# Performance work log

Hardware: AMD Instinct MI355X
Metric: run time of the kernel (lower is better)

Reference implementation:

```python
import jax, jax.numpy as jnp
import numpy as np

NUM_HEADS = 16
HIDDEN = 1024
TOTAL = 2048
NSEG = 8


def setup_inputs() -> dict:
    key = jax.random.key(0)
    ks = jax.random.split(key, 10)
    x = jax.random.normal(ks[0], (TOTAL, HIDDEN), dtype=jnp.float32)
    # cu_seqlens: [0, b1, ..., TOTAL], sorted segment boundaries
    inner = np.sort(np.random.default_rng(0).integers(1, TOTAL, size=NSEG - 1))
    cu_seqlens = jnp.asarray(np.concatenate([[0], inner, [TOTAL]]), dtype=jnp.int32)
    s = 1.0 / np.sqrt(HIDDEN)
    def lin(k):
        kw, kb = jax.random.split(k)
        W = jax.random.uniform(kw, (HIDDEN, HIDDEN), jnp.float32, -s, s)
        b = jax.random.uniform(kb, (HIDDEN,), jnp.float32, -s, s)
        return W, b
    Wq, bq = lin(ks[1]); Wk, bk = lin(ks[2]); Wv, bv = lin(ks[3]); Wo, bo = lin(ks[4])
    return {"hidden_states_packed": x, "cu_seqlens": cu_seqlens,
            "Wq": Wq, "bq": bq, "Wk": Wk, "bk": bk,
            "Wv": Wv, "bv": bv, "Wo": Wo, "bo": bo}


def reference(hidden_states_packed, cu_seqlens, Wq, bq, Wk, bk, Wv, bv, Wo, bo):
    T, H = hidden_states_packed.shape
    dh = H // NUM_HEADS
    x = hidden_states_packed
    q = (x @ Wq.T + bq).reshape(T, NUM_HEADS, dh)
    k = (x @ Wk.T + bk).reshape(T, NUM_HEADS, dh)
    v = (x @ Wv.T + bv).reshape(T, NUM_HEADS, dh)
    # segment id of each token from cu_seqlens boundaries
    seg = jnp.searchsorted(cu_seqlens, jnp.arange(T, dtype=jnp.int32), side="right")
    same_seg = seg[:, None] == seg[None, :]  # [T, T] block-diagonal mask
    scale = 1.0 / jnp.sqrt(jnp.asarray(dh, x.dtype))
    scores = jnp.einsum("qhd,khd->hqk", q, k) * scale  # [H, T, T]
    neg = jnp.asarray(jnp.finfo(scores.dtype).min, scores.dtype)
    scores = jnp.where(same_seg[None, :, :], scores, neg)
    attn = jax.nn.softmax(scores, axis=-1)
    ctx = jnp.einsum("hqk,khd->qhd", attn, v).reshape(T, H)
    return ctx @ Wo.T + bo
```

## Files before the change

kernel.cpp:

```cpp
#include <hip/hip_runtime.h>

typedef _Float16 f16x8 __attribute__((ext_vector_type(8)));
typedef _Float16 f16x4 __attribute__((ext_vector_type(4)));
typedef float    f32x4 __attribute__((ext_vector_type(4)));

#define MFMA_F16(a, b, c) __builtin_amdgcn_mfma_f32_16x16x32_f16((a), (b), (c), 0, 0, 0)

typedef __attribute__((address_space(1))) void gas_void;
typedef __attribute__((address_space(3))) void las_void;
#define GLOAD_LDS16(g, l) \
  __builtin_amdgcn_global_load_lds((gas_void*)(g), (las_void*)(l), 16, 0, 0)

#define NEG_INF (-__builtin_inff())

constexpr int T_SEQ  = 2048;
constexpr int HID    = 1024;
constexpr int NHEADS = 16;
constexpr int DH     = 64;
constexpr int NSEG   = 8;

__global__ __launch_bounds__(256) void convert_all(
    const float* __restrict__ x,
    const float* __restrict__ Wq, const float* __restrict__ Wk,
    const float* __restrict__ Wv, const float* __restrict__ Wo,
    _Float16* __restrict__ xh,
    _Float16* __restrict__ Wqh, _Float16* __restrict__ Wkh,
    _Float16* __restrict__ Wvh, _Float16* __restrict__ Woh) {
  int i = blockIdx.x * 256 + threadIdx.x;
  const float* src;
  _Float16* dst;
  int local;
  if (i < 524288) {
    src = x; dst = xh; local = i;
  } else {
    int j = i - 524288;
    int w = j >> 18;
    local = j & 262143;
    src = (w == 0) ? Wq : (w == 1) ? Wk : (w == 2) ? Wv : Wo;
    dst = (w == 0) ? Wqh : (w == 1) ? Wkh : (w == 2) ? Wvh : Woh;
  }
  float4 f = *(const float4*)(src + (size_t)local * 4);
  f16x4 h;
  h[0] = (_Float16)f.x; h[1] = (_Float16)f.y;
  h[2] = (_Float16)f.z; h[3] = (_Float16)f.w;
  *(f16x4*)(dst + (size_t)local * 4) = h;
}

template <int LAYOUT, int BM>
__device__ __forceinline__ void gemm128(const _Float16* __restrict__ A,
                                        const _Float16* __restrict__ B,
                                        const float* __restrict__ bias,
                                        _Float16* __restrict__ outh,
                                        float* __restrict__ outf) {
  constexpr int K = HID, N = HID;
  constexpr int MI = BM / 32;
  constexpr int LA = (BM * 8) / 512;
  __shared__ _Float16 As[BM * 64];
  __shared__ _Float16 Bs[128 * 64];
  const int tid  = threadIdx.x;
  const int wave = tid >> 6, lane = tid & 63;
  const int lr = lane & 15, lq = lane >> 4;
  const int wm = (wave >> 2) * (BM / 2);
  const int wn = (wave & 3) * 32;
  const int bm = blockIdx.y * BM, bn = blockIdx.x * 128;

  const _Float16* gA[LA > 0 ? LA : 1];
  const _Float16* gB[2];
  _Float16* lA[LA > 0 ? LA : 1];
  _Float16* lB[2];
#pragma unroll
  for (int i = 0; i < LA; ++i) {
    const int s = i * 512 + tid;
    const int row = s >> 3, pch = s & 7;
    const int lch = pch ^ (row & 7);
    gA[i] = A + (size_t)(bm + row) * K + lch * 8;
    lA[i] = &As[(i * 512 + wave * 64) * 8];
  }
#pragma unroll
  for (int i = 0; i < 2; ++i) {
    const int s = i * 512 + tid;
    const int row = s >> 3, pch = s & 7;
    const int lch = pch ^ (row & 7);
    gB[i] = B + (size_t)(bn + row) * K + lch * 8;
    lB[i] = &Bs[(i * 512 + wave * 64) * 8];
  }

  f32x4 acc[MI][2] = {};

  for (int kk = 0; kk < K; kk += 64) {
#pragma unroll
    for (int i = 0; i < LA; ++i) GLOAD_LDS16(gA[i] + kk, lA[i]);
#pragma unroll
    for (int i = 0; i < 2; ++i) GLOAD_LDS16(gB[i] + kk, lB[i]);
    __syncthreads();
#pragma unroll
    for (int ks = 0; ks < 2; ++ks) {
      f16x8 af[MI], bf[2];
#pragma unroll
      for (int mi = 0; mi < MI; ++mi) {
        const int row = wm + mi * 16 + lr;
        af[mi] = *(const f16x8*)&As[row * 64 + (((ks * 4 + lq) ^ (row & 7)) * 8)];
      }
#pragma unroll
      for (int ni = 0; ni < 2; ++ni) {
        const int row = wn + ni * 16 + lr;
        bf[ni] = *(const f16x8*)&Bs[row * 64 + (((ks * 4 + lq) ^ (row & 7)) * 8)];
      }
#pragma unroll
      for (int mi = 0; mi < MI; ++mi)
#pragma unroll
        for (int ni = 0; ni < 2; ++ni)
          acc[mi][ni] = MFMA_F16(af[mi], bf[ni], acc[mi][ni]);
    }
    __syncthreads();
  }

#pragma unroll
  for (int ni = 0; ni < 2; ++ni) {
    const int col = bn + wn + ni * 16 + lr;
    const float bv = bias[col];
#pragma unroll
    for (int mi = 0; mi < MI; ++mi) {
      const f32x4 v = acc[mi][ni];
      const int row0 = bm + wm + mi * 16 + lq * 4;
      if (LAYOUT == 3) {
        f16x4 o;
#pragma unroll
        for (int r = 0; r < 4; ++r) o[r] = (_Float16)(v[r] + bv);
        *(f16x4*)&outh[(size_t)col * T_SEQ + row0] = o;
      } else {
#pragma unroll
        for (int r = 0; r < 4; ++r) {
          const int row = row0 + r;
          const float val = v[r] + bv;
          if (LAYOUT == 0)
            outh[((size_t)(col >> 6) * T_SEQ + row) * DH + (col & 63)] = (_Float16)val;
          else
            outf[(size_t)row * N + col] = val;
        }
      }
    }
  }
}

__global__ __launch_bounds__(512) void gemm_qkv(
    const _Float16* __restrict__ xh,
    const _Float16* __restrict__ Wqh, const _Float16* __restrict__ Wkh,
    const _Float16* __restrict__ Wvh,
    const float* __restrict__ bq, const float* __restrict__ bk,
    const float* __restrict__ bv,
    _Float16* __restrict__ qp, _Float16* __restrict__ kp,
    _Float16* __restrict__ vT) {
  const int z = blockIdx.z;
  if (z == 0) {
    gemm128<0, 128>(xh, Wqh, bq, qp, nullptr);
  } else if (z == 1) {
    gemm128<0, 128>(xh, Wkh, bk, kp, nullptr);
  } else {
    gemm128<3, 128>(xh, Wvh, bv, vT, nullptr);
  }
}

__global__ __launch_bounds__(512) void gemm_out(
    const _Float16* __restrict__ ctxh, const _Float16* __restrict__ Woh,
    const float* __restrict__ bo, float* __restrict__ out) {
  gemm128<1, 64>(ctxh, Woh, bo, nullptr, out);
}

__device__ __forceinline__ float redsum16(float v) {
  v += __shfl_xor(v, 1);
  v += __shfl_xor(v, 2);
  v += __shfl_xor(v, 4);
  v += __shfl_xor(v, 8);
  return v;
}

__global__ __launch_bounds__(512, 4) void attn_kernel(
    const _Float16* __restrict__ qp, const _Float16* __restrict__ kp,
    const _Float16* __restrict__ vT, const int* __restrict__ cu,
    _Float16* __restrict__ ctx) {
  constexpr float SCL2E = 0.125f * 1.44269504f;
  constexpr int PSTR = 72;
  __shared__ _Float16 Ks[2][64 * 64];
  __shared__ _Float16 Vs[2][64 * 64];
  __shared__ _Float16 Pl[8][16 * PSTR];
  __shared__ float mO[4][16][64];
  __shared__ float mL[4][16];
  const int h  = blockIdx.y;
  const int q0 = blockIdx.x * 64;
  const int tid = threadIdx.x, wave = tid >> 6, lane = tid & 63;
  const int lr = lane & 15, lq = lane >> 4;
  const int qsub = wave & 3, khalf = wave >> 2;
  const int qw = q0 + qsub * 16;

  int cs[NSEG + 1];
#pragma unroll
  for (int i = 0; i <= NSEG; ++i) cs[i] = cu[i];

  int sstart[4], send[4];
#pragma unroll
  for (int r = 0; r < 4; ++r) {
    const int row = qw + lq * 4 + r;
    sstart[r] = 0; send[r] = T_SEQ;
#pragma unroll
    for (int s = 0; s < NSEG; ++s)
      if (row >= cs[s] && row < cs[s + 1]) { sstart[r] = cs[s]; send[r] = cs[s + 1]; }
  }
  int klo = 0, khi = T_SEQ;
#pragma unroll
  for (int s = 0; s < NSEG; ++s) {
    if (q0 >= cs[s] && q0 < cs[s + 1]) klo = cs[s];
    if (q0 + 63 >= cs[s] && q0 + 63 < cs[s + 1]) khi = cs[s + 1];
  }
  klo &= ~63;
  const int range  = khi - klo;
  const int hlen   = ((range + 127) >> 7) << 6;
  const int nsteps = hlen >> 6;
  const int kstart = klo + khalf * hlen;

  const _Float16* qbase = qp + ((size_t)h * T_SEQ + qw + lr) * DH;
  const f16x8 qf0 = *(const f16x8*)(qbase + lq * 8);
  const f16x8 qf1 = *(const f16x8*)(qbase + 32 + lq * 8);

  const _Float16* kb = kp + (size_t)h * T_SEQ * DH;
  const _Float16* vb = vT + (size_t)h * DH * T_SEQ;

  const int ht = qsub * 64 + lane;
  int kRow[2], kCol[2], vRow[2], vCol[2];
  _Float16* lK[2];
  _Float16* lV[2];
#pragma unroll
  for (int i = 0; i < 2; ++i) {
    const int s = i * 256 + ht;
    const int row = s >> 3, pch = s & 7;
    const int lch = pch ^ (row & 7);
    kRow[i] = row; kCol[i] = lch * 8;
    vRow[i] = row; vCol[i] = lch * 8;
    lK[i] = &Ks[khalf][(i * 256 + qsub * 64) * 8];
    lV[i] = &Vs[khalf][(i * 256 + qsub * 64) * 8];
  }

  float lst[4] = {0.f, 0.f, 0.f, 0.f};
  f32x4 oacc[4];
#pragma unroll
  for (int c = 0; c < 4; ++c) oacc[c] = f32x4{0.f, 0.f, 0.f, 0.f};

  _Float16* pw = &Pl[wave][0];

  for (int s = 0; s < nsteps; ++s) {
    const int kt = kstart + s * 64;
#pragma unroll
    for (int i = 0; i < 2; ++i) {
      const int grow = min(kt + kRow[i], T_SEQ - 1);
      GLOAD_LDS16(kb + (size_t)grow * DH + kCol[i], lK[i]);
    }
#pragma unroll
    for (int i = 0; i < 2; ++i) {
      const int gcol = min(kt + vCol[i], T_SEQ - 8);
      GLOAD_LDS16(vb + (size_t)vRow[i] * T_SEQ + gcol, lV[i]);
    }
    __syncthreads();

    f32x4 sc[4];
#pragma unroll
    for (int n = 0; n < 4; ++n) {
      const int row = n * 16 + lr;
      const f16x8 kf0 =
          *(const f16x8*)&Ks[khalf][row * 64 + (((0 * 4 + lq) ^ (row & 7)) * 8)];
      const f16x8 kf1 =
          *(const f16x8*)&Ks[khalf][row * 64 + (((1 * 4 + lq) ^ (row & 7)) * 8)];
      sc[n] = f32x4{0.f, 0.f, 0.f, 0.f};
      sc[n] = MFMA_F16(qf0, kf0, sc[n]);
      sc[n] = MFMA_F16(qf1, kf1, sc[n]);
    }
#pragma unroll
    for (int r = 0; r < 4; ++r) {
      float p[4];
#pragma unroll
      for (int n = 0; n < 4; ++n) {
        const int col = kt + n * 16 + lr;
        const float vv =
            (col >= sstart[r] && col < send[r]) ? sc[n][r] * SCL2E : NEG_INF;
        p[n] = exp2f(vv);
      }
      lst[r] += (p[0] + p[1]) + (p[2] + p[3]);
      _Float16* pr = &pw[(lq * 4 + r) * PSTR + lr];
      pr[0]  = (_Float16)p[0];
      pr[16] = (_Float16)p[1];
      pr[32] = (_Float16)p[2];
      pr[48] = (_Float16)p[3];
    }
    const f16x8 pf0 = *(const f16x8*)&pw[lr * PSTR + lq * 8];
    const f16x8 pf1 = *(const f16x8*)&pw[lr * PSTR + 32 + lq * 8];
#pragma unroll
    for (int c = 0; c < 4; ++c) {
      const int row = c * 16 + lr;
      const f16x8 vf0 =
          *(const f16x8*)&Vs[khalf][row * 64 + (((0 * 4 + lq) ^ (row & 7)) * 8)];
      const f16x8 vf1 =
          *(const f16x8*)&Vs[khalf][row * 64 + (((1 * 4 + lq) ^ (row & 7)) * 8)];
      oacc[c] = MFMA_F16(pf0, vf0, oacc[c]);
      oacc[c] = MFMA_F16(pf1, vf1, oacc[c]);
    }
    __syncthreads();
  }

#pragma unroll
  for (int r = 0; r < 4; ++r) lst[r] = redsum16(lst[r]);

  if (khalf) {
#pragma unroll
    for (int c = 0; c < 4; ++c)
#pragma unroll
      for (int r = 0; r < 4; ++r)
        mO[qsub][lq * 4 + r][c * 16 + lr] = oacc[c][r];
    if (lr == 0) {
#pragma unroll
      for (int r = 0; r < 4; ++r) mL[qsub][lq * 4 + r] = lst[r];
    }
  }
  __syncthreads();
  if (!khalf) {
#pragma unroll
    for (int r = 0; r < 4; ++r) lst[r] += mL[qsub][lq * 4 + r];
#pragma unroll
    for (int c = 0; c < 4; ++c)
#pragma unroll
      for (int r = 0; r < 4; ++r) {
        const int row = qw + lq * 4 + r;
        const float val =
            (oacc[c][r] + mO[qsub][lq * 4 + r][c * 16 + lr]) / lst[r];
        ctx[(size_t)row * HID + h * DH + c * 16 + lr] = (_Float16)val;
      }
  }
}

extern "C" void kernel_launch(void* const* d_in, const int* in_sizes, int n_in,
                              void* d_out, int out_size, void* d_ws, size_t ws_size,
                              hipStream_t stream) {
  const float* x  = (const float*)d_in[0];
  const int* cu   = (const int*)d_in[1];
  const float* Wq = (const float*)d_in[2]; const float* bq = (const float*)d_in[3];
  const float* Wk = (const float*)d_in[4]; const float* bk = (const float*)d_in[5];
  const float* Wv = (const float*)d_in[6]; const float* bv = (const float*)d_in[7];
  const float* Wo = (const float*)d_in[8]; const float* bo = (const float*)d_in[9];
  float* out = (float*)d_out;

  char* ws = (char*)d_ws;
  _Float16* xh   = (_Float16*)(ws + (size_t)0);
  _Float16* Wqh  = (_Float16*)(ws + ((size_t)4 << 20));
  _Float16* Wkh  = (_Float16*)(ws + ((size_t)6 << 20));
  _Float16* Wvh  = (_Float16*)(ws + ((size_t)8 << 20));
  _Float16* Woh  = (_Float16*)(ws + ((size_t)10 << 20));
  _Float16* qp   = (_Float16*)(ws + ((size_t)12 << 20));
  _Float16* kp   = (_Float16*)(ws + ((size_t)16 << 20));
  _Float16* vT   = (_Float16*)(ws + ((size_t)20 << 20));
  _Float16* ctxh = (_Float16*)(ws + ((size_t)24 << 20));

  convert_all<<<6144, 256, 0, stream>>>(x, Wq, Wk, Wv, Wo, xh, Wqh, Wkh, Wvh, Woh);
  gemm_qkv<<<dim3(8, 16, 3), 512, 0, stream>>>(xh, Wqh, Wkh, Wvh, bq, bk, bv, qp, kp, vT);
  attn_kernel<<<dim3(T_SEQ / 64, NHEADS), 512, 0, stream>>>(qp, kp, vT, cu, ctxh);
  gemm_out<<<dim3(8, 32), 512, 0, stream>>>(ctxh, Woh, bo, out);
}
```

Measured before the change: 141.7 us.

## Split GEMM K dimension across wave halves with LDS reduction

Restructures the projection GEMMs into an intra-block split-K: the 8 waves split into two groups that each process half of K with their own LDS tiles. Each wave now computes a larger 2x2-quadrant tile (4 N fragments instead of 2), which raises MFMA work per LDS fragment load. The partial sums are reduced through shared memory before the bias add and store. Launch bounds now request 4 blocks per CU. The cost is a larger LDS footprint, an extra reduction and barrier, and more accumulator registers per wave.

```diff
diff --git a/kernel.cpp b/kernel.cpp
--- a/kernel.cpp
+++ b/kernel.cpp
@@ -47,103 +47,129 @@
 }
 
 template <int LAYOUT, int BM>
-__device__ __forceinline__ void gemm128(const _Float16* __restrict__ A,
+__device__ __forceinline__ void gemm_sk(const _Float16* __restrict__ A,
                                         const _Float16* __restrict__ B,
                                         const float* __restrict__ bias,
                                         _Float16* __restrict__ outh,
                                         float* __restrict__ outf) {
-  constexpr int K = HID, N = HID;
-  constexpr int MI = BM / 32;
-  constexpr int LA = (BM * 8) / 512;
-  __shared__ _Float16 As[BM * 64];
-  __shared__ _Float16 Bs[128 * 64];
+  constexpr int K = HID, N = HID, KH = K / 2;
+  constexpr int QM = BM / 2;
+  constexpr int MI = QM / 16;
+  constexpr int LA = BM / 32;
+  __shared__ _Float16 SMEM[2 * BM * 64 + 2 * 128 * 64];
+  _Float16* As = SMEM;
+  _Float16* Bs = SMEM + 2 * BM * 64;
   const int tid  = threadIdx.x;
   const int wave = tid >> 6, lane = tid & 63;
   const int lr = lane & 15, lq = lane >> 4;
-  const int wm = (wave >> 2) * (BM / 2);
-  const int wn = (wave & 3) * 32;
+  const int kh = wave >> 2, q = wave & 3;
+  const int wm = (q >> 1) * QM, wn = (q & 1) * 64;
   const int bm = blockIdx.y * BM, bn = blockIdx.x * 128;
 
-  const _Float16* gA[LA > 0 ? LA : 1];
-  const _Float16* gB[2];
-  _Float16* lA[LA > 0 ? LA : 1];
-  _Float16* lB[2];
+  const int hl = q * 64 + lane;
+  const _Float16* gA[LA];
+  const _Float16* gB[4];
+  _Float16* lA[LA];
+  _Float16* lB[4];
 #pragma unroll
   for (int i = 0; i < LA; ++i) {
-    const int s = i * 512 + tid;
+    const int s = i * 256 + hl;
     const int row = s >> 3, pch = s & 7;
     const int lch = pch ^ (row & 7);
-    gA[i] = A + (size_t)(bm + row) * K + lch * 8;
-    lA[i] = &As[(i * 512 + wave * 64) * 8];
-  }
-#pragma unroll
-  for (int i = 0; i < 2; ++i) {
-    const int s = i * 512 + tid;
+    gA[i] = A + (size_t)(bm + row) * K + kh * KH + lch * 8;
+    lA[i] = &As[(kh * BM * 64) + (i * 256 + q * 64) * 8];
+  }
+#pragma unroll
+  for (int i = 0; i < 4; ++i) {
+    const int s = i * 256 + hl;
     const int row = s >> 3, pch = s & 7;
     const int lch = pch ^ (row & 7);
-    gB[i] = B + (size_t)(bn + row) * K + lch * 8;
-    lB[i] = &Bs[(i * 512 + wave * 64) * 8];
-  }
-
-  f32x4 acc[MI][2] = {};
-
-  for (int kk = 0; kk < K; kk += 64) {
+    gB[i] = B + (size_t)(bn + row) * K + kh * KH + lch * 8;
+    lB[i] = &Bs[(kh * 128 * 64) + (i * 256 + q * 64) * 8];
+  }
+
+  f32x4 acc[MI][4] = {};
+
+  for (int kk = 0; kk < KH; kk += 64) {
 #pragma unroll
     for (int i = 0; i < LA; ++i) GLOAD_LDS16(gA[i] + kk, lA[i]);
 #pragma unroll
-    for (int i = 0; i < 2; ++i) GLOAD_LDS16(gB[i] + kk, lB[i]);
+    for (int i = 0; i < 4; ++i) GLOAD_LDS16(gB[i] + kk, lB[i]);
     __syncthreads();
 #pragma unroll
     for (int ks = 0; ks < 2; ++ks) {
-      f16x8 af[MI], bf[2];
+      f16x8 af[MI], bf[4];
 #pragma unroll
       for (int mi = 0; mi < MI; ++mi) {
         const int row = wm + mi * 16 + lr;
-        af[mi] = *(const f16x8*)&As[row * 64 + (((ks * 4 + lq) ^ (row & 7)) * 8)];
-      }
-#pragma unroll
-      for (int ni = 0; ni < 2; ++ni) {
+        af[mi] = *(const f16x8*)&As[(kh * BM * 64) + row * 64 +
+                                    (((ks * 4 + lq) ^ (row & 7)) * 8)];
+      }
+#pragma unroll
+      for (int ni = 0; ni < 4; ++ni) {
         const int row = wn + ni * 16 + lr;
-        bf[ni] = *(const f16x8*)&Bs[row * 64 + (((ks * 4 + lq) ^ (row & 7)) * 8)];
+        bf[ni] = *(const f16x8*)&Bs[(kh * 128 * 64) + row * 64 +
+                                    (((ks * 4 + lq) ^ (row & 7)) * 8)];
       }
 #pragma unroll
       for (int mi = 0; mi < MI; ++mi)
 #pragma unroll
-        for (int ni = 0; ni < 2; ++ni)
+        for (int ni = 0; ni < 4; ++ni)
           acc[mi][ni] = MFMA_F16(af[mi], bf[ni], acc[mi][ni]);
     }
     __syncthreads();
   }
 
-#pragma unroll
-  for (int ni = 0; ni < 2; ++ni) {
-    const int col = bn + wn + ni * 16 + lr;
-    const float bv = bias[col];
-#pragma unroll
-    for (int mi = 0; mi < MI; ++mi) {
-      const f32x4 v = acc[mi][ni];
-      const int row0 = bm + wm + mi * 16 + lq * 4;
-      if (LAYOUT == 3) {
-        f16x4 o;
-#pragma unroll
-        for (int r = 0; r < 4; ++r) o[r] = (_Float16)(v[r] + bv);
-        *(f16x4*)&outh[(size_t)col * T_SEQ + row0] = o;
-      } else {
-#pragma unroll
-        for (int r = 0; r < 4; ++r) {
-          const int row = row0 + r;
-          const float val = v[r] + bv;
-          if (LAYOUT == 0)
-            outh[((size_t)(col >> 6) * T_SEQ + row) * DH + (col & 63)] = (_Float16)val;
-          else
-            outf[(size_t)row * N + col] = val;
+  float* mbuf = (float*)SMEM;
+  if (kh) {
+#pragma unroll
+    for (int mi = 0; mi < MI; ++mi)
+#pragma unroll
+      for (int ni = 0; ni < 4; ++ni)
+        *(f32x4*)&mbuf[(((q * 64 + lane) * MI * 4) + mi * 4 + ni) * 4] =
+            acc[mi][ni];
+  }
+  __syncthreads();
+  if (!kh) {
+#pragma unroll
+    for (int mi = 0; mi < MI; ++mi)
+#pragma unroll
+      for (int ni = 0; ni < 4; ++ni) {
+        const f32x4 o =
+            *(const f32x4*)&mbuf[(((q * 64 + lane) * MI * 4) + mi * 4 + ni) * 4];
+        acc[mi][ni] += o;
+      }
+#pragma unroll
+    for (int ni = 0; ni < 4; ++ni) {
+      const int col = bn + wn + ni * 16 + lr;
+      const float bv = bias[col];
+#pragma unroll
+      for (int mi = 0; mi < MI; ++mi) {
+        const f32x4 v = acc[mi][ni];
+        const int row0 = bm + wm + mi * 16 + lq * 4;
+        if (LAYOUT == 3) {
+          f16x4 o;
+#pragma unroll
+          for (int r = 0; r < 4; ++r) o[r] = (_Float16)(v[r] + bv);
+          *(f16x4*)&outh[(size_t)col * T_SEQ + row0] = o;
+        } else {
+#pragma unroll
+          for (int r = 0; r < 4; ++r) {
+            const int row = row0 + r;
+            const float val = v[r] + bv;
+            if (LAYOUT == 0)
+              outh[((size_t)(col >> 6) * T_SEQ + row) * DH + (col & 63)] =
+                  (_Float16)val;
+            else
+              outf[(size_t)row * N + col] = val;
+          }
         }
       }
     }
   }
 }
 
-__global__ __launch_bounds__(512) void gemm_qkv(
+__global__ __launch_bounds__(512, 4) void gemm_qkv(
     const _Float16* __restrict__ xh,
     const _Float16* __restrict__ Wqh, const _Float16* __restrict__ Wkh,
     const _Float16* __restrict__ Wvh,
@@ -153,18 +179,18 @@
     _Float16* __restrict__ vT) {
   const int z = blockIdx.z;
   if (z == 0) {
-    gemm128<0, 128>(xh, Wqh, bq, qp, nullptr);
+    gemm_sk<0, 128>(xh, Wqh, bq, qp, nullptr);
   } else if (z == 1) {
-    gemm128<0, 128>(xh, Wkh, bk, kp, nullptr);
+    gemm_sk<0, 128>(xh, Wkh, bk, kp, nullptr);
   } else {
-    gemm128<3, 128>(xh, Wvh, bv, vT, nullptr);
-  }
-}
-
-__global__ __launch_bounds__(512) void gemm_out(
+    gemm_sk<3, 128>(xh, Wvh, bv, vT, nullptr);
+  }
+}
+
+__global__ __launch_bounds__(512, 4) void gemm_out(
     const _Float16* __restrict__ ctxh, const _Float16* __restrict__ Woh,
     const float* __restrict__ bo, float* __restrict__ out) {
-  gemm128<1, 64>(ctxh, Woh, bo, nullptr, out);
+  gemm_sk<1, 64>(ctxh, Woh, bo, nullptr, out);
 }
 
 __device__ __forceinline__ float redsum16(float v) {
```

Result: slower. 157.5 us (+11.2%).
